# Kernel tuning notes

Measured on AMD Instinct MI355X. Metric: run time of the kernel, lower is better.

## Reference

```python
import jax, jax.numpy as jnp
import numpy as np

B, H, S, D, KG = 1, 8, 1024, 64, 10

def setup_inputs() -> dict:
    key = jax.random.key(0)
    ks = jax.random.split(key, 16)
    n = jax.random.normal
    u = jax.random.uniform
    return {
        'Q': n(ks[0], (B, H, S, D), dtype=jnp.float32),
        'K': n(ks[1], (B, H, S, D), dtype=jnp.float32),
        'V': n(ks[2], (B, H, S, D), dtype=jnp.float32),
        'distance_matrix': u(ks[3], (B, H, S, S), dtype=jnp.float32) * 10.0,
        'energy_matrix': u(ks[4], (B, H, S, S), dtype=jnp.float32) * 5.0,
        'mask': jnp.ones((B, H, S, S), dtype=jnp.int32),
        'mu_D': n(ks[5], (KG,), dtype=jnp.float32),
        'sigma_D': u(ks[6], (KG,), dtype=jnp.float32) + 0.5,  # keep sigma positive
        'b_D': n(ks[7], (KG,), dtype=jnp.float32) * 0.1,
        'mu_E': n(ks[8], (KG,), dtype=jnp.float32),
        'sigma_E': u(ks[9], (KG,), dtype=jnp.float32) + 0.5,
        'b_E': n(ks[10], (KG,), dtype=jnp.float32) * 0.1,
        'W1': n(ks[11], (KG, KG), dtype=jnp.float32) / np.sqrt(KG),
        'b1': jnp.zeros((KG,), dtype=jnp.float32),
        'W2': n(ks[12], (1, KG), dtype=jnp.float32) / np.sqrt(KG),
        'b2': jnp.zeros((1,), dtype=jnp.float32),
    }


def _rbf_mlp_bias(x, b, mu, sigma, W1, b1, W2, b2):
    # x: [B,H,S,S] -> Gaussian RBF features over K kernels, then small MLP -> [B,H,S,S]
    z = (x[..., None] + b - mu) / sigma                      # [B,H,S,S,K]
    inv_norm = 1.0 / (jnp.sqrt(2.0 * jnp.pi) * sigma)
    psi = jnp.exp(-0.5 * z * z) * inv_norm                   # [B,H,S,S,K]
    h = jax.nn.gelu(jnp.einsum('bhijk,lk->bhijl', psi, W1) + b1, approximate=False)
    return (jnp.einsum('bhijk,lk->bhijl', h, W2) + b2)[..., 0]


def reference(Q, K, V, distance_matrix, energy_matrix, mask,
              mu_D, sigma_D, b_D, mu_E, sigma_E, b_E, W1, b1, W2, b2):
    d_model = Q.shape[-1]
    scores = jnp.einsum('bhid,bhjd->bhij', Q, K) / np.sqrt(d_model * 2)
    scores = scores + _rbf_mlp_bias(distance_matrix, b_D, mu_D, sigma_D, W1, b1, W2, b2)
    scores = scores + _rbf_mlp_bias(energy_matrix, b_E, mu_E, sigma_E, W1, b1, W2, b2)
    scores = jnp.where(mask == 0, jnp.float32(-1e9), scores)
    attn = jax.nn.softmax(scores, axis=-1)
    return jnp.einsum('bhij,bhjd->bhid', attn, V)
```

## Files before the change

### kernel.cpp

```cpp
#include <hip/hip_runtime.h>
#include <math.h>

#define Hn 8
#define Sn 1024
#define Dn 64
#define KG 10

#define TN 2048
#define RD 10.25f
#define RE 5.125f

#define KS 4
#define NP (KS * 4)

typedef __attribute__((ext_vector_type(8))) short bf16x8;
typedef __attribute__((ext_vector_type(4))) float f32x4;
typedef unsigned short u16;
typedef unsigned int u32;

__device__ inline float bf2f(u16 u) {
    union { u32 i; float f; } v;
    v.i = ((u32)u) << 16;
    return v.f;
}

__device__ inline u16 f2bf(float f) {
    union { float f; u32 i; } v;
    v.f = f;
    u32 i = v.i;
    return (u16)((i + 0x7FFFu + ((i >> 16) & 1u)) >> 16);
}

__device__ float bias_eval(float x,
                           const float* __restrict__ mu, const float* __restrict__ sg,
                           const float* __restrict__ bb,
                           const float* __restrict__ W1, const float* __restrict__ b1,
                           const float* __restrict__ W2, const float* __restrict__ b2) {
    const float inv_s2pi = 0.39894228040143267794f;
    float psi[KG];
#pragma unroll
    for (int k = 0; k < KG; k++) {
        float s = sg[k];
        float z = (x + bb[k] - mu[k]) / s;
        psi[k] = __expf(-0.5f * z * z) * (inv_s2pi / s);
    }
    float out = b2[0];
#pragma unroll
    for (int l = 0; l < KG; l++) {
        float a = b1[l];
#pragma unroll
        for (int k = 0; k < KG; k++) a += psi[k] * W1[l * KG + k];
        float g = 0.5f * a * (1.0f + erff(a * 0.70710678118654752440f));
        out += g * W2[l];
    }
    return out;
}

#define QK4 262144
#define VTN 524288

__global__ __launch_bounds__(256) void prep_kernel(
    const float* __restrict__ Q, const float* __restrict__ K, const float* __restrict__ V,
    const float* __restrict__ muD, const float* __restrict__ sgD, const float* __restrict__ bD,
    const float* __restrict__ muE, const float* __restrict__ sgE, const float* __restrict__ bE,
    const float* __restrict__ W1, const float* __restrict__ b1,
    const float* __restrict__ W2, const float* __restrict__ b2,
    u32* __restrict__ tab, u16* __restrict__ Qb, u16* __restrict__ Kb, u16* __restrict__ VTi)
{
    int id = blockIdx.x * 256 + threadIdx.x;
    if (id < 2 * TN) {
        int which = (id >= TN);
        int idx = id & (TN - 1);
        float h = (which ? RE : RD) / (float)TN;
        float x0 = idx * h;
        float v0, v1;
        if (which) {
            v0 = bias_eval(x0,     muE, sgE, bE, W1, b1, W2, b2);
            v1 = bias_eval(x0 + h, muE, sgE, bE, W1, b1, W2, b2);
        } else {
            v0 = bias_eval(x0,     muD, sgD, bD, W1, b1, W2, b2);
            v1 = bias_eval(x0 + h, muD, sgD, bD, W1, b1, W2, b2);
        }
        tab[id] = (u32)f2bf(v0) | ((u32)f2bf(v1 - v0) << 16);
    } else if (id < 2 * TN + QK4) {
        int i = id - 2 * TN;
        int arr = i >> 17;
        i &= (1 << 17) - 1;
        float4 v = ((const float4*)(arr ? K : Q))[i];
        ushort4 o;
        o.x = f2bf(v.x); o.y = f2bf(v.y); o.z = f2bf(v.z); o.w = f2bf(v.w);
        ((ushort4*)(arr ? Kb : Qb))[i] = o;
    } else if (id < 2 * TN + QK4 + VTN) {
        int g = id - (2 * TN + QK4);
        int h = g >> 16;
        int d = (g >> 10) & 63;
        int s = g & 1023;
        int t = s >> 5, q = (s >> 3) & 3, j = s & 7;
        int src_s = (t << 5) + (q << 2) + (j & 3) + ((j >> 2) << 4);
        VTi[g] = f2bf(V[(((size_t)h << 10) + src_s) * Dn + d]);
    }
}

__device__ inline float lerp_tab(const u32* __restrict__ st, float x, float invh) {
    float tf = x * invh;
    int i = (int)tf;
    i = max(0, min(i, TN - 1));
    float fr = tf - (float)i;
    u32 p = st[i];
    return fmaf(bf2f((u16)(p >> 16)), fr, bf2f((u16)p));
}

__global__ __launch_bounds__(256, 8) void attn_kernel(
    const u16* __restrict__ Qb, const u16* __restrict__ Kb, const u16* __restrict__ VTi,
    const float* __restrict__ Dm, const float* __restrict__ Em, const int* __restrict__ Mk,
    const u32* __restrict__ gtab,
    float* __restrict__ Up, float* __restrict__ Mp, float* __restrict__ Lp)
{
    __shared__ __align__(16) u32 sTab[2 * TN];

    const int tid = threadIdx.x;
    {
        const uint4* g4 = (const uint4*)gtab;
        uint4* s4 = (uint4*)sTab;
#pragma unroll
        for (int i = 0; i < 4; i++) s4[tid + 256 * i] = g4[tid + 256 * i];
    }
    __syncthreads();

    const int h    = blockIdx.y;
    const int qb   = blockIdx.x;
    const int ks   = blockIdx.z;
    const int q0   = qb * 16;
    const int wave = tid >> 6;
    const int lane = tid & 63;
    const int quad = lane >> 4;
    const int l16  = lane & 15;

    const u16* Qh = Qb  + (size_t)h * Sn * Dn;
    const u16* Kh = Kb  + (size_t)h * Sn * Dn;
    const u16* Vh = VTi + (size_t)h * Dn * Sn;
    const float* Dh = Dm + (size_t)h * Sn * Sn + (size_t)(q0 + l16) * Sn;
    const float* Eh = Em + (size_t)h * Sn * Sn + (size_t)(q0 + l16) * Sn;
    const int*   Mh = Mk + (size_t)h * Sn * Sn + (size_t)(q0 + l16) * Sn;
    const float invhD = (float)TN / RD;
    const float invhE = (float)TN / RE;
    const float scale = 0.08838834764831845f;

    const bf16x8 bQ0 = *(const bf16x8*)(Qh + (q0 + l16) * Dn + quad * 8);
    const bf16x8 bQ1 = *(const bf16x8*)(Qh + (q0 + l16) * Dn + 32 + quad * 8);

    f32x4 O0 = {0.f, 0.f, 0.f, 0.f}, O1 = O0, O2 = O0, O3 = O0;
    float m_run = -1e30f, l_run = 0.f;

    for (int t = 0; t < 2; t++) {
        const int k0 = ks * 256 + wave * 64 + t * 32;

        const float4 Dv0 = *(const float4*)(Dh + k0 + quad * 4);
        const float4 Dv1 = *(const float4*)(Dh + k0 + 16 + quad * 4);
        const float4 Ev0 = *(const float4*)(Eh + k0 + quad * 4);
        const float4 Ev1 = *(const float4*)(Eh + k0 + 16 + quad * 4);
        const int4   Mv0 = *(const int4*)(Mh + k0 + quad * 4);
        const int4   Mv1 = *(const int4*)(Mh + k0 + 16 + quad * 4);

        const u16* kr = Kh + (size_t)(k0 + l16) * Dn + quad * 8;
        const bf16x8 aK00 = *(const bf16x8*)(kr);
        const bf16x8 aK01 = *(const bf16x8*)(kr + 32);
        const bf16x8 aK10 = *(const bf16x8*)(kr + 16 * Dn);
        const bf16x8 aK11 = *(const bf16x8*)(kr + 16 * Dn + 32);

        const u16* vr = Vh + k0 + quad * 8;
        const bf16x8 bV0 = *(const bf16x8*)(vr + (size_t)(l16)      * Sn);
        const bf16x8 bV1 = *(const bf16x8*)(vr + (size_t)(16 + l16) * Sn);
        const bf16x8 bV2 = *(const bf16x8*)(vr + (size_t)(32 + l16) * Sn);
        const bf16x8 bV3 = *(const bf16x8*)(vr + (size_t)(48 + l16) * Sn);

        f32x4 s0 = {0.f, 0.f, 0.f, 0.f}, s1 = s0;
        s0 = __builtin_amdgcn_mfma_f32_16x16x32_bf16(aK00, bQ0, s0, 0, 0, 0);
        s0 = __builtin_amdgcn_mfma_f32_16x16x32_bf16(aK01, bQ1, s0, 0, 0, 0);
        s1 = __builtin_amdgcn_mfma_f32_16x16x32_bf16(aK10, bQ0, s1, 0, 0, 0);
        s1 = __builtin_amdgcn_mfma_f32_16x16x32_bf16(aK11, bQ1, s1, 0, 0, 0);

        const float dv0[4] = {Dv0.x, Dv0.y, Dv0.z, Dv0.w};
        const float dv1[4] = {Dv1.x, Dv1.y, Dv1.z, Dv1.w};
        const float ev0[4] = {Ev0.x, Ev0.y, Ev0.z, Ev0.w};
        const float ev1[4] = {Ev1.x, Ev1.y, Ev1.z, Ev1.w};
        const int   mv0[4] = {Mv0.x, Mv0.y, Mv0.z, Mv0.w};
        const int   mv1[4] = {Mv1.x, Mv1.y, Mv1.z, Mv1.w};

        float sc0[4], sc1[4];
#pragma unroll
        for (int r = 0; r < 4; r++) {
            float v0 = s0[r] * scale + lerp_tab(sTab, dv0[r], invhD)
                                     + lerp_tab(sTab + TN, ev0[r], invhE);
            v0 = fminf(fmaxf(v0, -80.f), 80.f);
            sc0[r] = (mv0[r] == 0) ? -1e9f : v0;
            float v1 = s1[r] * scale + lerp_tab(sTab, dv1[r], invhD)
                                     + lerp_tab(sTab + TN, ev1[r], invhE);
            v1 = fminf(fmaxf(v1, -80.f), 80.f);
            sc1[r] = (mv1[r] == 0) ? -1e9f : v1;
        }

        float mloc = fmaxf(fmaxf(fmaxf(sc0[0], sc0[1]), fmaxf(sc0[2], sc0[3])),
                           fmaxf(fmaxf(sc1[0], sc1[1]), fmaxf(sc1[2], sc1[3])));
        mloc = fmaxf(mloc, __shfl_xor(mloc, 16, 64));
        mloc = fmaxf(mloc, __shfl_xor(mloc, 32, 64));

        const float mn = fmaxf(m_run, mloc);
        const float al = __expf(m_run - mn);
        m_run = mn;

        float p0[4], p1[4], ll = 0.f;
#pragma unroll
        for (int r = 0; r < 4; r++) {
            p0[r] = __expf(sc0[r] - mn);
            p1[r] = __expf(sc1[r] - mn);
            ll += p0[r] + p1[r];
        }
        ll += __shfl_xor(ll, 16, 64);
        ll += __shfl_xor(ll, 32, 64);
        l_run = l_run * al + ll;

        bf16x8 aP;
#pragma unroll
        for (int r = 0; r < 4; r++) {
            aP[r]     = (short)f2bf(p0[r]);
            aP[4 + r] = (short)f2bf(p1[r]);
        }

        const float a0 = __shfl(al, quad * 4 + 0, 64);
        const float a1 = __shfl(al, quad * 4 + 1, 64);
        const float a2 = __shfl(al, quad * 4 + 2, 64);
        const float a3 = __shfl(al, quad * 4 + 3, 64);
        O0[0] *= a0; O0[1] *= a1; O0[2] *= a2; O0[3] *= a3;
        O1[0] *= a0; O1[1] *= a1; O1[2] *= a2; O1[3] *= a3;
        O2[0] *= a0; O2[1] *= a1; O2[2] *= a2; O2[3] *= a3;
        O3[0] *= a0; O3[1] *= a1; O3[2] *= a2; O3[3] *= a3;

        O0 = __builtin_amdgcn_mfma_f32_16x16x32_bf16(aP, bV0, O0, 0, 0, 0);
        O1 = __builtin_amdgcn_mfma_f32_16x16x32_bf16(aP, bV1, O1, 0, 0, 0);
        O2 = __builtin_amdgcn_mfma_f32_16x16x32_bf16(aP, bV2, O2, 0, 0, 0);
        O3 = __builtin_amdgcn_mfma_f32_16x16x32_bf16(aP, bV3, O3, 0, 0, 0);
    }

    const int p = ks * 4 + wave;
    const size_t pg = (size_t)(h * 64 + qb) * NP + p;
    float* up = Up + pg * 16 * 64;
#pragma unroll
    for (int r = 0; r < 4; r++) {
        const int row = quad * 4 + r;
        up[row * 64 +  0 + l16] = O0[r];
        up[row * 64 + 16 + l16] = O1[r];
        up[row * 64 + 32 + l16] = O2[r];
        up[row * 64 + 48 + l16] = O3[r];
    }
    if (lane < 16) {
        Mp[pg * 16 + lane] = m_run;
        Lp[pg * 16 + lane] = l_run;
    }
}

__global__ __launch_bounds__(256) void combine_kernel(
    const float* __restrict__ Up, const float* __restrict__ Mp,
    const float* __restrict__ Lp, float* __restrict__ out)
{
    const int g  = blockIdx.x * 256 + threadIdx.x;
    const int r  = g >> 4;
    const int c4 = (g & 15) * 4;
    const int h  = r >> 10;
    const int s  = r & 1023;
    const int qb = s >> 4;
    const int r16 = s & 15;
    const size_t pg0 = (size_t)(h * 64 + qb) * NP;

    float m[NP], l[NP];
#pragma unroll
    for (int k = 0; k < NP; k++) {
        m[k] = Mp[(pg0 + k) * 16 + r16];
        l[k] = Lp[(pg0 + k) * 16 + r16];
    }
    float M = m[0];
#pragma unroll
    for (int k = 1; k < NP; k++) M = fmaxf(M, m[k]);
    float f[NP], L = 0.f;
#pragma unroll
    for (int k = 0; k < NP; k++) {
        f[k] = __expf(m[k] - M);
        L += l[k] * f[k];
    }
    const float inv = 1.0f / L;

    float acc[4] = {0.f, 0.f, 0.f, 0.f};
#pragma unroll
    for (int k = 0; k < NP; k++) {
        const float4 u = *(const float4*)(Up + ((pg0 + k) * 16 + r16) * 64 + c4);
        acc[0] += u.x * f[k]; acc[1] += u.y * f[k];
        acc[2] += u.z * f[k]; acc[3] += u.w * f[k];
    }
    float4 ov = {acc[0] * inv, acc[1] * inv, acc[2] * inv, acc[3] * inv};
    *(float4*)(out + (size_t)r * Dn + c4) = ov;
}

extern "C" void kernel_launch(void* const* d_in, const int* in_sizes, int n_in,
                              void* d_out, int out_size, void* d_ws, size_t ws_size,
                              hipStream_t stream) {
    const float* Q    = (const float*)d_in[0];
    const float* K    = (const float*)d_in[1];
    const float* V    = (const float*)d_in[2];
    const float* Dm   = (const float*)d_in[3];
    const float* Em   = (const float*)d_in[4];
    const int*   Mask = (const int*)d_in[5];
    const float* muD  = (const float*)d_in[6];
    const float* sgD  = (const float*)d_in[7];
    const float* bD   = (const float*)d_in[8];
    const float* muE  = (const float*)d_in[9];
    const float* sgE  = (const float*)d_in[10];
    const float* bE   = (const float*)d_in[11];
    const float* W1   = (const float*)d_in[12];
    const float* b1   = (const float*)d_in[13];
    const float* W2   = (const float*)d_in[14];
    const float* b2   = (const float*)d_in[15];

    u32* tab = (u32*)d_ws;
    u16* Qb  = (u16*)((char*)d_ws + 2 * TN * 4);
    u16* Kb  = Qb + (size_t)Hn * Sn * Dn;
    u16* VTi = Kb + (size_t)Hn * Sn * Dn;
    float* Up = (float*)(VTi + (size_t)Hn * Sn * Dn);
    float* Mp = Up + (size_t)Hn * 64 * NP * 16 * 64;
    float* Lp = Mp + (size_t)Hn * 64 * NP * 16;

    const int prep_threads = 2 * TN + QK4 + VTN;
    prep_kernel<<<prep_threads / 256, 256, 0, stream>>>(
        Q, K, V, muD, sgD, bD, muE, sgE, bE, W1, b1, W2, b2,
        tab, Qb, Kb, VTi);

    dim3 grid(Sn / 16, Hn, KS);
    attn_kernel<<<grid, 256, 0, stream>>>(Qb, Kb, VTi, Dm, Em, Mask, tab,
                                          Up, Mp, Lp);

    combine_kernel<<<(Hn * Sn * 16) / 256, 256, 0, stream>>>(Up, Mp, Lp,
                                                             (float*)d_out);
}
```

Baseline: 191.0 us.

## Stage K/V and bias tiles through double-buffered LDS with wider query blocks

Each block now covers 64 queries (16 per wave), and every wave walks all 256 keys of its split in eight 32-key steps. K, V and the distance, energy and mask tiles are staged into a double-buffered LDS area with async global-to-LDS loads, so the next tile loads while the current one is computed. This shares K/V across waves and cuts the softmax partials per row from 16 to 4, which shrinks the combine kernel's work. The cost is about 80KB of LDS per block, a barrier every step, and a four-times smaller grid, which lowers occupancy and latency hiding.

```diff
diff --git a/kernel.cpp b/kernel.cpp
--- a/kernel.cpp
+++ b/kernel.cpp
@@ -11,7 +11,6 @@
 #define RE 5.125f
 
 #define KS 4
-#define NP (KS * 4)
 
 typedef __attribute__((ext_vector_type(8))) short bf16x8;
 typedef __attribute__((ext_vector_type(4))) float f32x4;
@@ -29,6 +28,13 @@
     v.f = f;
     u32 i = v.i;
     return (u16)((i + 0x7FFFu + ((i >> 16) & 1u)) >> 16);
+}
+
+__device__ inline void stage16(const void* g, void* l) {
+    __builtin_amdgcn_global_load_lds(
+        (const __attribute__((address_space(1))) unsigned int*)g,
+        (__attribute__((address_space(3))) unsigned int*)l,
+        16, 0, 0);
 }
 
 __device__ float bias_eval(float x,
@@ -110,13 +116,16 @@
     return fmaf(bf2f((u16)(p >> 16)), fr, bf2f((u16)p));
 }
 
-__global__ __launch_bounds__(256, 8) void attn_kernel(
+#define BUFSZ 32768
+
+__global__ __launch_bounds__(256) void attn_kernel(
     const u16* __restrict__ Qb, const u16* __restrict__ Kb, const u16* __restrict__ VTi,
     const float* __restrict__ Dm, const float* __restrict__ Em, const int* __restrict__ Mk,
     const u32* __restrict__ gtab,
     float* __restrict__ Up, float* __restrict__ Mp, float* __restrict__ Lp)
 {
     __shared__ __align__(16) u32 sTab[2 * TN];
+    __shared__ __align__(16) char sBuf[2 * BUFSZ];
 
     const int tid = threadIdx.x;
     {
@@ -125,16 +134,16 @@
 #pragma unroll
         for (int i = 0; i < 4; i++) s4[tid + 256 * i] = g4[tid + 256 * i];
     }
-    __syncthreads();
 
     const int h    = blockIdx.y;
     const int qb   = blockIdx.x;
     const int ks   = blockIdx.z;
-    const int q0   = qb * 16;
     const int wave = tid >> 6;
     const int lane = tid & 63;
     const int quad = lane >> 4;
     const int l16  = lane & 15;
+    const int q0   = qb * 64 + wave * 16;
+    const int kbase = ks * 256;
 
     const u16* Qh = Qb  + (size_t)h * Sn * Dn;
     const u16* Kh = Kb  + (size_t)h * Sn * Dn;
@@ -149,30 +158,57 @@
     const bf16x8 bQ0 = *(const bf16x8*)(Qh + (q0 + l16) * Dn + quad * 8);
     const bf16x8 bQ1 = *(const bf16x8*)(Qh + (q0 + l16) * Dn + 32 + quad * 8);
 
+#define STAGE(bufp, tt) do {                                                   \
+        const int k0_ = kbase + (tt) * 32;                                     \
+        char* b_ = (bufp);                                                     \
+        if (wave < 2) {                                                        \
+            const u16* kr_ = Kh + (size_t)(k0_ + l16 + wave * 16) * Dn + quad * 8; \
+            stage16(kr_,      b_ + wave * 2048);                               \
+            stage16(kr_ + 32, b_ + wave * 2048 + 1024);                        \
+        } else {                                                               \
+            const int c_ = (wave - 2) * 2;                                     \
+            const u16* vr_ = Vh + k0_ + quad * 8 + (size_t)(l16 + 16 * c_) * Sn; \
+            stage16(vr_,           b_ + 4096 + c_ * 1024);                     \
+            stage16(vr_ + 16 * Sn, b_ + 4096 + c_ * 1024 + 1024);              \
+        }                                                                      \
+        const float* dr_ = Dh + k0_ + quad * 4;                                \
+        const float* er_ = Eh + k0_ + quad * 4;                                \
+        const int*   mr_ = Mh + k0_ + quad * 4;                                \
+        char* w_ = b_ + 8192 + wave * 6144;                                    \
+        stage16(dr_,       w_);                                                \
+        stage16(dr_ + 16,  w_ + 1024);                                         \
+        stage16(er_,       w_ + 2048);                                         \
+        stage16(er_ + 16,  w_ + 3072);                                         \
+        stage16(mr_,       w_ + 4096);                                         \
+        stage16(mr_ + 16,  w_ + 5120);                                         \
+    } while (0)
+
     f32x4 O0 = {0.f, 0.f, 0.f, 0.f}, O1 = O0, O2 = O0, O3 = O0;
     float m_run = -1e30f, l_run = 0.f;
 
-    for (int t = 0; t < 2; t++) {
-        const int k0 = ks * 256 + wave * 64 + t * 32;
-
-        const float4 Dv0 = *(const float4*)(Dh + k0 + quad * 4);
-        const float4 Dv1 = *(const float4*)(Dh + k0 + 16 + quad * 4);
-        const float4 Ev0 = *(const float4*)(Eh + k0 + quad * 4);
-        const float4 Ev1 = *(const float4*)(Eh + k0 + 16 + quad * 4);
-        const int4   Mv0 = *(const int4*)(Mh + k0 + quad * 4);
-        const int4   Mv1 = *(const int4*)(Mh + k0 + 16 + quad * 4);
-
-        const u16* kr = Kh + (size_t)(k0 + l16) * Dn + quad * 8;
-        const bf16x8 aK00 = *(const bf16x8*)(kr);
-        const bf16x8 aK01 = *(const bf16x8*)(kr + 32);
-        const bf16x8 aK10 = *(const bf16x8*)(kr + 16 * Dn);
-        const bf16x8 aK11 = *(const bf16x8*)(kr + 16 * Dn + 32);
-
-        const u16* vr = Vh + k0 + quad * 8;
-        const bf16x8 bV0 = *(const bf16x8*)(vr + (size_t)(l16)      * Sn);
-        const bf16x8 bV1 = *(const bf16x8*)(vr + (size_t)(16 + l16) * Sn);
-        const bf16x8 bV2 = *(const bf16x8*)(vr + (size_t)(32 + l16) * Sn);
-        const bf16x8 bV3 = *(const bf16x8*)(vr + (size_t)(48 + l16) * Sn);
+    STAGE(sBuf, 0);
+    __syncthreads();
+
+    for (int t = 0; t < 8; t++) {
+        char* cur = sBuf + (t & 1) * BUFSZ;
+        if (t < 7) STAGE(sBuf + ((t & 1) ^ 1) * BUFSZ, t + 1);
+
+        const char* ls = cur + lane * 16;
+        const bf16x8 aK00 = *(const bf16x8*)(ls);
+        const bf16x8 aK01 = *(const bf16x8*)(ls + 1024);
+        const bf16x8 aK10 = *(const bf16x8*)(ls + 2048);
+        const bf16x8 aK11 = *(const bf16x8*)(ls + 3072);
+        const bf16x8 bV0  = *(const bf16x8*)(ls + 4096);
+        const bf16x8 bV1  = *(const bf16x8*)(ls + 5120);
+        const bf16x8 bV2  = *(const bf16x8*)(ls + 6144);
+        const bf16x8 bV3  = *(const bf16x8*)(ls + 7168);
+        const char* ld = cur + 8192 + wave * 6144 + lane * 16;
+        const float4 Dv0  = *(const float4*)(ld);
+        const float4 Dv1  = *(const float4*)(ld + 1024);
+        const float4 Ev0  = *(const float4*)(ld + 2048);
+        const float4 Ev1  = *(const float4*)(ld + 3072);
+        const int4   Mv0  = *(const int4*)(ld + 4096);
+        const int4   Mv1  = *(const int4*)(ld + 5120);
 
         f32x4 s0 = {0.f, 0.f, 0.f, 0.f}, s1 = s0;
         s0 = __builtin_amdgcn_mfma_f32_16x16x32_bf16(aK00, bQ0, s0, 0, 0, 0);
@@ -240,11 +276,13 @@
         O1 = __builtin_amdgcn_mfma_f32_16x16x32_bf16(aP, bV1, O1, 0, 0, 0);
         O2 = __builtin_amdgcn_mfma_f32_16x16x32_bf16(aP, bV2, O2, 0, 0, 0);
         O3 = __builtin_amdgcn_mfma_f32_16x16x32_bf16(aP, bV3, O3, 0, 0, 0);
-    }
-
-    const int p = ks * 4 + wave;
-    const size_t pg = (size_t)(h * 64 + qb) * NP + p;
-    float* up = Up + pg * 16 * 64;
+
+        __syncthreads();
+    }
+#undef STAGE
+
+    const int pb = (h * 64 + qb * 4 + wave) * KS + ks;
+    float* up = Up + (size_t)pb * 1024;
 #pragma unroll
     for (int r = 0; r < 4; r++) {
         const int row = quad * 4 + r;
@@ -254,8 +292,8 @@
         up[row * 64 + 48 + l16] = O3[r];
     }
     if (lane < 16) {
-        Mp[pg * 16 + lane] = m_run;
-        Lp[pg * 16 + lane] = l_run;
+        Mp[pb * 16 + lane] = m_run;
+        Lp[pb * 16 + lane] = l_run;
     }
 }
 
@@ -268,22 +306,22 @@
     const int c4 = (g & 15) * 4;
     const int h  = r >> 10;
     const int s  = r & 1023;
-    const int qb = s >> 4;
+    const int qt = s >> 4;
     const int r16 = s & 15;
-    const size_t pg0 = (size_t)(h * 64 + qb) * NP;
-
-    float m[NP], l[NP];
-#pragma unroll
-    for (int k = 0; k < NP; k++) {
-        m[k] = Mp[(pg0 + k) * 16 + r16];
-        l[k] = Lp[(pg0 + k) * 16 + r16];
+    const int pb0 = (h * 64 + qt) * KS;
+
+    float m[KS], l[KS];
+#pragma unroll
+    for (int k = 0; k < KS; k++) {
+        m[k] = Mp[(pb0 + k) * 16 + r16];
+        l[k] = Lp[(pb0 + k) * 16 + r16];
     }
     float M = m[0];
 #pragma unroll
-    for (int k = 1; k < NP; k++) M = fmaxf(M, m[k]);
-    float f[NP], L = 0.f;
-#pragma unroll
-    for (int k = 0; k < NP; k++) {
+    for (int k = 1; k < KS; k++) M = fmaxf(M, m[k]);
+    float f[KS], L = 0.f;
+#pragma unroll
+    for (int k = 0; k < KS; k++) {
         f[k] = __expf(m[k] - M);
         L += l[k] * f[k];
     }
@@ -291,8 +329,8 @@
 
     float acc[4] = {0.f, 0.f, 0.f, 0.f};
 #pragma unroll
-    for (int k = 0; k < NP; k++) {
-        const float4 u = *(const float4*)(Up + ((pg0 + k) * 16 + r16) * 64 + c4);
+    for (int k = 0; k < KS; k++) {
+        const float4 u = *(const float4*)(Up + (size_t)(pb0 + k) * 1024 + r16 * 64 + c4);
         acc[0] += u.x * f[k]; acc[1] += u.y * f[k];
         acc[2] += u.z * f[k]; acc[3] += u.w * f[k];
     }
@@ -325,15 +363,15 @@
     u16* Kb  = Qb + (size_t)Hn * Sn * Dn;
     u16* VTi = Kb + (size_t)Hn * Sn * Dn;
     float* Up = (float*)(VTi + (size_t)Hn * Sn * Dn);
-    float* Mp = Up + (size_t)Hn * 64 * NP * 16 * 64;
-    float* Lp = Mp + (size_t)Hn * 64 * NP * 16;
+    float* Mp = Up + (size_t)Hn * 64 * KS * 16 * 64;
+    float* Lp = Mp + (size_t)Hn * 64 * KS * 16;
 
     const int prep_threads = 2 * TN + QK4 + VTN;
     prep_kernel<<<prep_threads / 256, 256, 0, stream>>>(
         Q, K, V, muD, sgD, bD, muE, sgE, bE, W1, b1, W2, b2,
         tab, Qb, Kb, VTi);
 
-    dim3 grid(Sn / 16, Hn, KS);
+    dim3 grid(Sn / 64, Hn, KS);
     attn_kernel<<<grid, 256, 0, stream>>>(Qb, Kb, VTi, Dm, Em, Mask, tab,
                                           Up, Mp, Lp);
 
```

After: 173.4 us. 9.2% less time.
